# Performance work log

Hardware: AMD Instinct MI355X
Metric: run time of the kernel (lower is better)

Reference implementation:

```python
import jax, jax.numpy as jnp
import numpy as np

B, T, D, NH = 2, 2048, 1024, 32
HD = D // NH  # 32
EPS = 1e-6


def rms_norm(x):
    # normalize over head dim in fp32, cast back
    ms = jnp.mean(x.astype(jnp.float32) ** 2, axis=-1, keepdims=True)
    return x * jax.lax.rsqrt(ms + EPS).astype(x.dtype)


def apply_rope(x, cos, sin):
    d = x.shape[-1] // 2
    x1, x2 = x[..., :d], x[..., d:]
    c = cos[: x.shape[-2], :d]
    s = sin[: x.shape[-2], :d]
    return jnp.concatenate([x1 * c - x2 * s, x2 * c + x1 * s], axis=-1)


def setup_inputs() -> dict:
    key = jax.random.key(0)
    ks = jax.random.split(key, 5)
    sc = 1.0 / np.sqrt(D)
    x = jax.random.normal(ks[0], (B, T, D), jnp.float32)
    Wq = jax.random.normal(ks[1], (D, D), jnp.float32) * sc
    Wk = jax.random.normal(ks[2], (NH * HD, D), jnp.float32) * sc
    Wv = jax.random.normal(ks[3], (NH * HD, D), jnp.float32) * sc
    Wproj = jax.random.normal(ks[4], (D, D), jnp.float32) * sc
    q_gain = jnp.ones((NH,), jnp.float32)  # qk_gain = 1.0
    # real RoPE tables, shape [T, HD//2]
    pos = np.arange(T, dtype=np.float32)
    inv = 1.0 / (10000.0 ** (np.arange(HD // 2, dtype=np.float32) / (HD // 2)))
    ang = pos[:, None] * inv[None, :]
    cos = jnp.asarray(np.cos(ang), jnp.float32)
    sin = jnp.asarray(np.sin(ang), jnp.float32)
    return {"x": x, "Wq": Wq, "Wk": Wk, "Wv": Wv, "Wproj": Wproj,
            "q_gain": q_gain, "cos": cos, "sin": sin}


def reference(x, Wq, Wk, Wv, Wproj, q_gain, cos, sin):
    Bx, Tx, Dx = x.shape
    nh = q_gain.shape[0]
    hd = Dx // nh
    # projections -> [B, H, T, hd]
    q = (x @ Wq.T).reshape(Bx, Tx, nh, hd).transpose(0, 2, 1, 3)
    k = (x @ Wk.T).reshape(Bx, Tx, nh, hd).transpose(0, 2, 1, 3)
    v = (x @ Wv.T).reshape(Bx, Tx, nh, hd).transpose(0, 2, 1, 3)
    q = apply_rope(rms_norm(q), cos, sin) * q_gain[None, :, None, None]
    k = apply_rope(rms_norm(k), cos, sin)
    scale = hd ** (-0.5)
    scores = jnp.einsum('bhqd,bhkd->bhqk', q, k) * scale
    causal = jnp.tril(jnp.ones((Tx, Tx), bool))
    scores = jnp.where(causal, scores, jnp.finfo(scores.dtype).min)
    attn = jax.nn.softmax(scores, axis=-1)
    y = jnp.einsum('bhqk,bhkd->bhqd', attn, v)
    y = y.transpose(0, 2, 1, 3).reshape(Bx, Tx, Dx)
    return y @ Wproj.T
```

## Files before the change

### kernel.cpp

```cpp
#include <hip/hip_runtime.h>

#define DEV __device__ __forceinline__

typedef __bf16 bf16x8 __attribute__((ext_vector_type(8)));
typedef float f32x4 __attribute__((ext_vector_type(4)));

static constexpr int Tn = 2048;
static constexpr int Dn = 1024;
static constexpr int NHn = 32;
static constexpr int Mn = 2 * Tn;
static constexpr float QSCALE = 0.17677669529663687f * 1.4426950408889634f;

DEV unsigned short f2bf(float f) {
    unsigned int u = __builtin_bit_cast(unsigned int, f);
    u = u + 0x7FFFu + ((u >> 16) & 1u);
    return (unsigned short)(u >> 16);
}

#define GPTR(p) ((const __attribute__((address_space(1))) void*)(p))
#define LPTR(p) ((__attribute__((address_space(3))) void*)(p))

__global__ __launch_bounds__(256) void cast_all(
    const float* __restrict__ x, const float* __restrict__ Wq, const float* __restrict__ Wk,
    const float* __restrict__ Wv, const float* __restrict__ Wp,
    unsigned short* __restrict__ xb, unsigned short* __restrict__ wall) {
    int i = blockIdx.x * 256 + threadIdx.x;
    const float* src;
    ushort4* dst;
    if (i < (1 << 20)) {
        src = x + (size_t)i * 4;
        dst = reinterpret_cast<ushort4*>(xb) + i;
    } else {
        int j = i - (1 << 20);
        int sel = j >> 18, off = j & ((1 << 18) - 1);
        const float* w = (sel == 0) ? Wq : (sel == 1) ? Wk : (sel == 2) ? Wv : Wp;
        src = w + (size_t)off * 4;
        dst = reinterpret_cast<ushort4*>(wall) + ((size_t)sel << 18) + off;
    }
    float4 v = *reinterpret_cast<const float4*>(src);
    ushort4 o;
    o.x = f2bf(v.x); o.y = f2bf(v.y); o.z = f2bf(v.z); o.w = f2bf(v.w);
    *dst = o;
}

__global__ __launch_bounds__(256) void gemm_qkv(
    const unsigned short* __restrict__ A, const unsigned short* __restrict__ Wall,
    unsigned short* __restrict__ Qn, unsigned short* __restrict__ Kn, unsigned short* __restrict__ Vt,
    const float* __restrict__ gain, const float* __restrict__ cosp, const float* __restrict__ sinp) {
    const int z = blockIdx.z;
    const unsigned short* Bm = Wall + (size_t)z * (Dn * Dn);
    const int m0 = blockIdx.x * 128, n0 = blockIdx.y * 128;
    const int tid = threadIdx.x, w = tid >> 6, l = tid & 63;
    const int wm = w & 1, wn = w >> 1, lm = l & 15, quad = l >> 4;

    __shared__ __align__(16) unsigned short As[128 * 32];
    __shared__ __align__(16) unsigned short Bs[128 * 32];

    f32x4 acc[4][4] = {};

    const int r0 = (w * 2 + 0) * 16 + (l >> 2);
    const int r1 = (w * 2 + 1) * 16 + (l >> 2);
    const int c0 = (l & 3) * 8;
    const unsigned short* gA0 = A + (long)(m0 + r0) * Dn + c0;
    const unsigned short* gA1 = A + (long)(m0 + r1) * Dn + c0;
    const unsigned short* gB0 = Bm + (long)(n0 + r0) * Dn + c0;
    const unsigned short* gB1 = Bm + (long)(n0 + r1) * Dn + c0;
    unsigned short* lA0 = As + (w * 2 + 0) * 16 * 32;
    unsigned short* lA1 = As + (w * 2 + 1) * 16 * 32;
    unsigned short* lB0 = Bs + (w * 2 + 0) * 16 * 32;
    unsigned short* lB1 = Bs + (w * 2 + 1) * 16 * 32;

    for (int kk = 0; kk < Dn; kk += 32) {
        __builtin_amdgcn_global_load_lds(GPTR(gA0 + kk), LPTR(lA0), 16, 0, 0);
        __builtin_amdgcn_global_load_lds(GPTR(gA1 + kk), LPTR(lA1), 16, 0, 0);
        __builtin_amdgcn_global_load_lds(GPTR(gB0 + kk), LPTR(lB0), 16, 0, 0);
        __builtin_amdgcn_global_load_lds(GPTR(gB1 + kk), LPTR(lB1), 16, 0, 0);
        __syncthreads();
        bf16x8 af[4], bfv[4];
#pragma unroll
        for (int mt = 0; mt < 4; ++mt)
            af[mt] = __builtin_bit_cast(bf16x8,
                *reinterpret_cast<const uint4*>(As + (wm * 64 + mt * 16 + lm) * 32 + quad * 8));
#pragma unroll
        for (int nt = 0; nt < 4; ++nt)
            bfv[nt] = __builtin_bit_cast(bf16x8,
                *reinterpret_cast<const uint4*>(Bs + (wn * 64 + nt * 16 + lm) * 32 + quad * 8));
#pragma unroll
        for (int mt = 0; mt < 4; ++mt)
#pragma unroll
            for (int nt = 0; nt < 4; ++nt)
                acc[mt][nt] = __builtin_amdgcn_mfma_f32_16x16x32_bf16(af[mt], bfv[nt], acc[mt][nt], 0, 0, 0);
        __syncthreads();
    }

    if (z == 2) {
#pragma unroll
        for (int mt = 0; mt < 4; ++mt) {
            int row0 = m0 + wm * 64 + mt * 16 + quad * 4;
            int b_ = row0 >> 11, t_ = row0 & (Tn - 1);
#pragma unroll
            for (int nt = 0; nt < 4; ++nt) {
                int col = n0 + wn * 64 + nt * 16 + lm;
                int hh = col >> 5, dd = col & 31;
                ushort4 o4;
                o4.x = f2bf(acc[mt][nt][0]); o4.y = f2bf(acc[mt][nt][1]);
                o4.z = f2bf(acc[mt][nt][2]); o4.w = f2bf(acc[mt][nt][3]);
                *reinterpret_cast<ushort4*>(&Vt[((long)(b_ * NHn + hh) * 32 + dd) * Tn + t_]) = o4;
            }
        }
    } else {
        unsigned short* dst = z ? Kn : Qn;
#pragma unroll
        for (int mt = 0; mt < 4; ++mt)
#pragma unroll
            for (int r = 0; r < 4; ++r) {
                int row = m0 + wm * 64 + mt * 16 + quad * 4 + r;
                int b_ = row >> 11, t_ = row & (Tn - 1);
                float c = cosp[t_ * 16 + lm], s = sinp[t_ * 16 + lm];
#pragma unroll
                for (int g = 0; g < 2; ++g) {
                    float x1 = acc[mt][2 * g][r], x2 = acc[mt][2 * g + 1][r];
                    float ssv = x1 * x1 + x2 * x2;
#pragma unroll
                    for (int off = 8; off >= 1; off >>= 1) ssv += __shfl_xor(ssv, off, 16);
                    float rinv = rsqrtf(ssv * (1.0f / 32.0f) + 1e-6f);
                    x1 *= rinv; x2 *= rinv;
                    float o1 = x1 * c - x2 * s;
                    float o2 = x2 * c + x1 * s;
                    int hh = (n0 + wn * 64 + g * 32) >> 5;
                    if (z == 0) { float gs = gain[hh] * QSCALE; o1 *= gs; o2 *= gs; }
                    long base = ((long)(b_ * NHn + hh) * Tn + t_) * 32;
                    dst[base + lm] = f2bf(o1);
                    dst[base + 16 + lm] = f2bf(o2);
                }
            }
    }
}

__global__ __launch_bounds__(256) void gemm_proj(
    const unsigned short* __restrict__ A, const unsigned short* __restrict__ Bm,
    float* __restrict__ C) {
    const int m0 = blockIdx.x * 128, n0 = blockIdx.y * 128;
    const int tid = threadIdx.x, w = tid >> 6, l = tid & 63;
    const int wm = w & 1, wn = w >> 1, lm = l & 15, quad = l >> 4;

    __shared__ __align__(16) unsigned short As[128 * 32];
    __shared__ __align__(16) unsigned short Bs[128 * 32];

    f32x4 acc[4][4] = {};

    const int r0 = (w * 2 + 0) * 16 + (l >> 2);
    const int r1 = (w * 2 + 1) * 16 + (l >> 2);
    const int c0 = (l & 3) * 8;
    const unsigned short* gA0 = A + (long)(m0 + r0) * Dn + c0;
    const unsigned short* gA1 = A + (long)(m0 + r1) * Dn + c0;
    const unsigned short* gB0 = Bm + (long)(n0 + r0) * Dn + c0;
    const unsigned short* gB1 = Bm + (long)(n0 + r1) * Dn + c0;
    unsigned short* lA0 = As + (w * 2 + 0) * 16 * 32;
    unsigned short* lA1 = As + (w * 2 + 1) * 16 * 32;
    unsigned short* lB0 = Bs + (w * 2 + 0) * 16 * 32;
    unsigned short* lB1 = Bs + (w * 2 + 1) * 16 * 32;

    for (int kk = 0; kk < Dn; kk += 32) {
        __builtin_amdgcn_global_load_lds(GPTR(gA0 + kk), LPTR(lA0), 16, 0, 0);
        __builtin_amdgcn_global_load_lds(GPTR(gA1 + kk), LPTR(lA1), 16, 0, 0);
        __builtin_amdgcn_global_load_lds(GPTR(gB0 + kk), LPTR(lB0), 16, 0, 0);
        __builtin_amdgcn_global_load_lds(GPTR(gB1 + kk), LPTR(lB1), 16, 0, 0);
        __syncthreads();
        bf16x8 af[4], bfv[4];
#pragma unroll
        for (int mt = 0; mt < 4; ++mt)
            af[mt] = __builtin_bit_cast(bf16x8,
                *reinterpret_cast<const uint4*>(As + (wm * 64 + mt * 16 + lm) * 32 + quad * 8));
#pragma unroll
        for (int nt = 0; nt < 4; ++nt)
            bfv[nt] = __builtin_bit_cast(bf16x8,
                *reinterpret_cast<const uint4*>(Bs + (wn * 64 + nt * 16 + lm) * 32 + quad * 8));
#pragma unroll
        for (int mt = 0; mt < 4; ++mt)
#pragma unroll
            for (int nt = 0; nt < 4; ++nt)
                acc[mt][nt] = __builtin_amdgcn_mfma_f32_16x16x32_bf16(af[mt], bfv[nt], acc[mt][nt], 0, 0, 0);
        __syncthreads();
    }
#pragma unroll
    for (int mt = 0; mt < 4; ++mt)
#pragma unroll
        for (int nt = 0; nt < 4; ++nt)
#pragma unroll
            for (int r = 0; r < 4; ++r) {
                int rg = m0 + wm * 64 + mt * 16 + quad * 4 + r;
                int cg = n0 + wn * 64 + nt * 16 + lm;
                C[(long)rg * Dn + cg] = acc[mt][nt][r];
            }
}

__global__ __launch_bounds__(256) void attn(
    const unsigned short* __restrict__ Qn, const unsigned short* __restrict__ Kn,
    const unsigned short* __restrict__ Vt, unsigned short* __restrict__ Y) {
    const int bx = blockIdx.x, h = blockIdx.y, b = blockIdx.z;
    const int tid = threadIdx.x, w = tid >> 6, l = tid & 63;
    const int lm = l & 15, quad = l >> 4;
    const long bh = b * NHn + h;
    const unsigned short* Qh = Qn + bh * Tn * 32;
    const unsigned short* Kh = Kn + bh * Tn * 32;
    const unsigned short* Vh = Vt + bh * 32 * Tn;
    __shared__ __align__(16) unsigned short Pl[4][16][76];
    unsigned short* Pw = &Pl[w][0][0];

    for (int pass = 0; pass < 2; ++pass) {
        const int qb = pass ? (15 - bx) : bx;
        const int q0 = qb * 128 + w * 32;

        bf16x8 qf[2];
        float negM[2][4];
        float lpart[2][4] = {};
        f32x4 o[2][2] = {{{0.f, 0.f, 0.f, 0.f}, {0.f, 0.f, 0.f, 0.f}},
                         {{0.f, 0.f, 0.f, 0.f}, {0.f, 0.f, 0.f, 0.f}}};
#pragma unroll
        for (int t = 0; t < 2; ++t) {
            qf[t] = __builtin_bit_cast(bf16x8,
                *reinterpret_cast<const uint4*>(Qh + (q0 + t * 16 + lm) * 32 + quad * 8));
            float ss = 0.f;
#pragma unroll
            for (int j = 0; j < 8; ++j) { float v = (float)qf[t][j]; ss += v * v; }
            ss += __shfl_xor(ss, 16);
            ss += __shfl_xor(ss, 32);
            float Mv = __builtin_sqrtf(ss * 32.0f);
#pragma unroll
            for (int r = 0; r < 4; ++r) negM[t][r] = -__shfl(Mv, quad * 4 + r, 16);
        }

        const int kend = q0 + 31;
        uint4 ka[4], va[4], kb2[4], vb2[4];

        auto load_t = [&](uint4* kd, uint4* vd, int k0) {
#pragma unroll
            for (int i = 0; i < 4; ++i)
                kd[i] = *reinterpret_cast<const uint4*>(Kh + (k0 + i * 16 + lm) * 32 + quad * 8);
#pragma unroll
            for (int kf2 = 0; kf2 < 2; ++kf2)
#pragma unroll
                for (int nh_ = 0; nh_ < 2; ++nh_)
                    vd[kf2 * 2 + nh_] = *reinterpret_cast<const uint4*>(
                        Vh + (nh_ * 16 + lm) * Tn + k0 + kf2 * 32 + quad * 8);
        };

        auto compute_t = [&](const uint4* kd, const uint4* vd, int k0) {
#pragma unroll
            for (int t = 0; t < 2; ++t) {
                if (k0 > q0 + t * 16 + 15) continue;
                f32x4 s[4];
#pragma unroll
                for (int i = 0; i < 4; ++i) {
                    f32x4 zz = {0.f, 0.f, 0.f, 0.f};
                    s[i] = __builtin_amdgcn_mfma_f32_16x16x32_bf16(
                        qf[t], __builtin_bit_cast(bf16x8, kd[i]), zz, 0, 0, 0);
                }
                const bool full = (k0 + 63) <= (q0 + t * 16);
#pragma unroll
                for (int r = 0; r < 4; ++r) {
                    const int qrow = q0 + t * 16 + quad * 4 + r;
                    const float nm = negM[t][r];
                    float ls = lpart[t][r];
#pragma unroll
                    for (int i = 0; i < 4; ++i) {
                        float p = __builtin_amdgcn_exp2f(s[i][r] + nm);
                        if (!full) {
                            int kc = k0 + i * 16 + lm;
                            p = (kc <= qrow) ? p : 0.0f;
                        }
                        s[i][r] = p;
                        ls += p;
                    }
                    lpart[t][r] = ls;
                }
#pragma unroll
                for (int i = 0; i < 4; ++i)
#pragma unroll
                    for (int r = 0; r < 4; ++r)
                        Pw[(quad * 4 + r) * 76 + i * 16 + lm] = f2bf(s[i][r]);
#pragma unroll
                for (int kf2 = 0; kf2 < 2; ++kf2) {
                    bf16x8 pf = __builtin_bit_cast(bf16x8,
                        *reinterpret_cast<const uint4*>(Pw + lm * 76 + kf2 * 32 + quad * 8));
#pragma unroll
                    for (int nh_ = 0; nh_ < 2; ++nh_)
                        o[t][nh_] = __builtin_amdgcn_mfma_f32_16x16x32_bf16(
                            pf, __builtin_bit_cast(bf16x8, vd[kf2 * 2 + nh_]), o[t][nh_], 0, 0, 0);
                }
            }
        };

        load_t(ka, va, 0);
        int k0 = 0;
        while (true) {
            int nk = k0 + 64;
            if (nk <= kend) load_t(kb2, vb2, nk);
            compute_t(ka, va, k0);
            if (nk > kend) break;
            k0 = nk;
            nk = k0 + 64;
            if (nk <= kend) load_t(ka, va, nk);
            compute_t(kb2, vb2, k0);
            if (nk > kend) break;
            k0 = nk;
        }

#pragma unroll
        for (int t = 0; t < 2; ++t)
#pragma unroll
            for (int r = 0; r < 4; ++r) {
                float ls = lpart[t][r];
#pragma unroll
                for (int off = 8; off >= 1; off >>= 1) ls += __shfl_xor(ls, off, 16);
                float inv = 1.0f / ls;
                int qrow = q0 + t * 16 + quad * 4 + r;
                long base = ((long)(b * Tn + qrow) * NHn + h) * 32;
                Y[base + lm] = f2bf(o[t][0][r] * inv);
                Y[base + 16 + lm] = f2bf(o[t][1][r] * inv);
            }
    }
}

extern "C" void kernel_launch(void* const* d_in, const int* in_sizes, int n_in,
                              void* d_out, int out_size, void* d_ws, size_t ws_size,
                              hipStream_t stream) {
    (void)in_sizes; (void)n_in; (void)out_size; (void)ws_size;
    const float* x = (const float*)d_in[0];
    const float* Wq = (const float*)d_in[1];
    const float* Wk = (const float*)d_in[2];
    const float* Wv = (const float*)d_in[3];
    const float* Wp = (const float*)d_in[4];
    const float* gain = (const float*)d_in[5];
    const float* cosp = (const float*)d_in[6];
    const float* sinp = (const float*)d_in[7];

    char* ws = (char*)d_ws;
    const size_t SZ = (size_t)Mn * Dn * 2;
    unsigned short* xb = (unsigned short*)ws;
    unsigned short* wall = (unsigned short*)(ws + SZ);
    unsigned short* qn = (unsigned short*)(ws + 2 * SZ);
    unsigned short* kn = qn + (size_t)Mn * Dn;
    unsigned short* vt = kn + (size_t)Mn * Dn;
    unsigned short* ybuf = vt + (size_t)Mn * Dn;

    cast_all<<<8192, 256, 0, stream>>>(x, Wq, Wk, Wv, Wp, xb, wall);

    gemm_qkv<<<dim3(Mn / 128, Dn / 128, 3), 256, 0, stream>>>(
        xb, wall, qn, kn, vt, gain, cosp, sinp);

    attn<<<dim3(8, NHn, 2), 256, 0, stream>>>(qn, kn, vt, ybuf);

    gemm_proj<<<dim3(Mn / 128, Dn / 128), 256, 0, stream>>>(
        ybuf, wall + (size_t)3 * Dn * Dn, (float*)d_out);
}
```

Baseline: 213.4 us.

## Shrink attention query tile to 16 rows per wave and double the grid

The attention kernel now gives each wave 16 query rows instead of 32 and each block 64 rows instead of 128, and doubles the grid to 16x32x2 blocks. The row-max offset is folded into the QK MFMA accumulator input, which removes an add before each exp2. Launch bounds now request 4 blocks per CU, and the bf16 conversion uses the compiler's native cast. The aim is more parallelism, better occupancy and less causal load imbalance, at the cost of reloading K/V twice as often per query row.

```diff
diff --git a/kernel.cpp b/kernel.cpp
--- a/kernel.cpp
+++ b/kernel.cpp
@@ -12,9 +12,7 @@
 static constexpr float QSCALE = 0.17677669529663687f * 1.4426950408889634f;
 
 DEV unsigned short f2bf(float f) {
-    unsigned int u = __builtin_bit_cast(unsigned int, f);
-    u = u + 0x7FFFu + ((u >> 16) & 1u);
-    return (unsigned short)(u >> 16);
+    return __builtin_bit_cast(unsigned short, (__bf16)f);
 }
 
 #define GPTR(p) ((const __attribute__((address_space(1))) void*)(p))
@@ -195,7 +193,7 @@
             }
 }
 
-__global__ __launch_bounds__(256) void attn(
+__global__ __launch_bounds__(256, 4) void attn(
     const unsigned short* __restrict__ Qn, const unsigned short* __restrict__ Kn,
     const unsigned short* __restrict__ Vt, unsigned short* __restrict__ Y) {
     const int bx = blockIdx.x, h = blockIdx.y, b = blockIdx.z;
@@ -209,29 +207,25 @@
     unsigned short* Pw = &Pl[w][0][0];
 
     for (int pass = 0; pass < 2; ++pass) {
-        const int qb = pass ? (15 - bx) : bx;
-        const int q0 = qb * 128 + w * 32;
-
-        bf16x8 qf[2];
-        float negM[2][4];
-        float lpart[2][4] = {};
-        f32x4 o[2][2] = {{{0.f, 0.f, 0.f, 0.f}, {0.f, 0.f, 0.f, 0.f}},
-                         {{0.f, 0.f, 0.f, 0.f}, {0.f, 0.f, 0.f, 0.f}}};
-#pragma unroll
-        for (int t = 0; t < 2; ++t) {
-            qf[t] = __builtin_bit_cast(bf16x8,
-                *reinterpret_cast<const uint4*>(Qh + (q0 + t * 16 + lm) * 32 + quad * 8));
-            float ss = 0.f;
-#pragma unroll
-            for (int j = 0; j < 8; ++j) { float v = (float)qf[t][j]; ss += v * v; }
-            ss += __shfl_xor(ss, 16);
-            ss += __shfl_xor(ss, 32);
-            float Mv = __builtin_sqrtf(ss * 32.0f);
-#pragma unroll
-            for (int r = 0; r < 4; ++r) negM[t][r] = -__shfl(Mv, quad * 4 + r, 16);
-        }
-
-        const int kend = q0 + 31;
+        const int qt = pass ? (31 - bx) : bx;
+        const int q0 = qt * 64 + w * 16;
+
+        bf16x8 qf = __builtin_bit_cast(bf16x8,
+            *reinterpret_cast<const uint4*>(Qh + (q0 + lm) * 32 + quad * 8));
+        float ss = 0.f;
+#pragma unroll
+        for (int j = 0; j < 8; ++j) { float v = (float)qf[j]; ss += v * v; }
+        ss += __shfl_xor(ss, 16);
+        ss += __shfl_xor(ss, 32);
+        float Mv = __builtin_sqrtf(ss * 32.0f);
+        f32x4 negM;
+#pragma unroll
+        for (int r = 0; r < 4; ++r) negM[r] = -__shfl(Mv, quad * 4 + r, 16);
+
+        float lpart[4] = {};
+        f32x4 o[2] = {{0.f, 0.f, 0.f, 0.f}, {0.f, 0.f, 0.f, 0.f}};
+
+        const int kend = q0 + 15;
         uint4 ka[4], va[4], kb2[4], vb2[4];
 
         auto load_t = [&](uint4* kd, uint4* vd, int k0) {
@@ -247,48 +241,41 @@
         };
 
         auto compute_t = [&](const uint4* kd, const uint4* vd, int k0) {
-#pragma unroll
-            for (int t = 0; t < 2; ++t) {
-                if (k0 > q0 + t * 16 + 15) continue;
-                f32x4 s[4];
+            f32x4 s[4];
+#pragma unroll
+            for (int i = 0; i < 4; ++i)
+                s[i] = __builtin_amdgcn_mfma_f32_16x16x32_bf16(
+                    qf, __builtin_bit_cast(bf16x8, kd[i]), negM, 0, 0, 0);
+            const bool full = (k0 + 63) <= q0;
+#pragma unroll
+            for (int r = 0; r < 4; ++r) {
+                const int qrow = q0 + quad * 4 + r;
+                float ls = lpart[r];
 #pragma unroll
                 for (int i = 0; i < 4; ++i) {
-                    f32x4 zz = {0.f, 0.f, 0.f, 0.f};
-                    s[i] = __builtin_amdgcn_mfma_f32_16x16x32_bf16(
-                        qf[t], __builtin_bit_cast(bf16x8, kd[i]), zz, 0, 0, 0);
+                    float p = __builtin_amdgcn_exp2f(s[i][r]);
+                    if (!full) {
+                        int kc = k0 + i * 16 + lm;
+                        p = (kc <= qrow) ? p : 0.0f;
+                    }
+                    s[i][r] = p;
+                    ls += p;
                 }
-                const bool full = (k0 + 63) <= (q0 + t * 16);
-#pragma unroll
-                for (int r = 0; r < 4; ++r) {
-                    const int qrow = q0 + t * 16 + quad * 4 + r;
-                    const float nm = negM[t][r];
-                    float ls = lpart[t][r];
-#pragma unroll
-                    for (int i = 0; i < 4; ++i) {
-                        float p = __builtin_amdgcn_exp2f(s[i][r] + nm);
-                        if (!full) {
-                            int kc = k0 + i * 16 + lm;
-                            p = (kc <= qrow) ? p : 0.0f;
-                        }
-                        s[i][r] = p;
-                        ls += p;
-                    }
-                    lpart[t][r] = ls;
-                }
-#pragma unroll
-                for (int i = 0; i < 4; ++i)
-#pragma unroll
-                    for (int r = 0; r < 4; ++r)
-                        Pw[(quad * 4 + r) * 76 + i * 16 + lm] = f2bf(s[i][r]);
-#pragma unroll
-                for (int kf2 = 0; kf2 < 2; ++kf2) {
-                    bf16x8 pf = __builtin_bit_cast(bf16x8,
-                        *reinterpret_cast<const uint4*>(Pw + lm * 76 + kf2 * 32 + quad * 8));
-#pragma unroll
-                    for (int nh_ = 0; nh_ < 2; ++nh_)
-                        o[t][nh_] = __builtin_amdgcn_mfma_f32_16x16x32_bf16(
-                            pf, __builtin_bit_cast(bf16x8, vd[kf2 * 2 + nh_]), o[t][nh_], 0, 0, 0);
-                }
+                lpart[r] = ls;
+            }
+#pragma unroll
+            for (int i = 0; i < 4; ++i)
+#pragma unroll
+                for (int r = 0; r < 4; ++r)
+                    Pw[(quad * 4 + r) * 76 + i * 16 + lm] = f2bf(s[i][r]);
+#pragma unroll
+            for (int kf2 = 0; kf2 < 2; ++kf2) {
+                bf16x8 pf = __builtin_bit_cast(bf16x8,
+                    *reinterpret_cast<const uint4*>(Pw + lm * 76 + kf2 * 32 + quad * 8));
+#pragma unroll
+                for (int nh_ = 0; nh_ < 2; ++nh_)
+                    o[nh_] = __builtin_amdgcn_mfma_f32_16x16x32_bf16(
+                        pf, __builtin_bit_cast(bf16x8, vd[kf2 * 2 + nh_]), o[nh_], 0, 0, 0);
             }
         };
 
@@ -308,18 +295,16 @@
         }
 
 #pragma unroll
-        for (int t = 0; t < 2; ++t)
-#pragma unroll
-            for (int r = 0; r < 4; ++r) {
-                float ls = lpart[t][r];
-#pragma unroll
-                for (int off = 8; off >= 1; off >>= 1) ls += __shfl_xor(ls, off, 16);
-                float inv = 1.0f / ls;
-                int qrow = q0 + t * 16 + quad * 4 + r;
-                long base = ((long)(b * Tn + qrow) * NHn + h) * 32;
-                Y[base + lm] = f2bf(o[t][0][r] * inv);
-                Y[base + 16 + lm] = f2bf(o[t][1][r] * inv);
-            }
+        for (int r = 0; r < 4; ++r) {
+            float ls = lpart[r];
+#pragma unroll
+            for (int off = 8; off >= 1; off >>= 1) ls += __shfl_xor(ls, off, 16);
+            float inv = 1.0f / ls;
+            int qrow = q0 + quad * 4 + r;
+            long base = ((long)(b * Tn + qrow) * NHn + h) * 32;
+            Y[base + lm] = f2bf(o[0][r] * inv);
+            Y[base + 16 + lm] = f2bf(o[1][r] * inv);
+        }
     }
 }
 
@@ -350,7 +335,7 @@
     gemm_qkv<<<dim3(Mn / 128, Dn / 128, 3), 256, 0, stream>>>(
         xb, wall, qn, kn, vt, gain, cosp, sinp);
 
-    attn<<<dim3(8, NHn, 2), 256, 0, stream>>>(qn, kn, vt, ybuf);
+    attn<<<dim3(16, NHn, 2), 256, 0, stream>>>(qn, kn, vt, ybuf);
 
     gemm_proj<<<dim3(Mn / 128, Dn / 128), 256, 0, stream>>>(
         ybuf, wall + (size_t)3 * Dn * Dn, (float*)d_out);
```

New measurement: 270.8 us. +26.9%, slower.

## Split attention key range across two wave groups and merge partials in LDS

Applied to the files above, without the earlier changes.

The attention kernel now launches 512 threads per block. Two groups of four waves each process half of the causal key tiles for the same query rows, and the partial outputs and row sums are combined through shared memory before the write. The per-row max subtraction is folded into the MFMA accumulator init, and f2bf uses the native bf16 conversion. This raises parallelism per block to shorten the critical path of long causal rows. The cost is extra shared memory and two block barriers per pass.

```diff
diff --git a/kernel.cpp b/kernel.cpp
--- a/kernel.cpp
+++ b/kernel.cpp
@@ -12,9 +12,7 @@
 static constexpr float QSCALE = 0.17677669529663687f * 1.4426950408889634f;
 
 DEV unsigned short f2bf(float f) {
-    unsigned int u = __builtin_bit_cast(unsigned int, f);
-    u = u + 0x7FFFu + ((u >> 16) & 1u);
-    return (unsigned short)(u >> 16);
+    return __builtin_bit_cast(unsigned short, (__bf16)f);
 }
 
 #define GPTR(p) ((const __attribute__((address_space(1))) void*)(p))
@@ -195,25 +193,27 @@
             }
 }
 
-__global__ __launch_bounds__(256) void attn(
+__global__ __launch_bounds__(512, 4) void attn(
     const unsigned short* __restrict__ Qn, const unsigned short* __restrict__ Kn,
     const unsigned short* __restrict__ Vt, unsigned short* __restrict__ Y) {
     const int bx = blockIdx.x, h = blockIdx.y, b = blockIdx.z;
     const int tid = threadIdx.x, w = tid >> 6, l = tid & 63;
+    const int wq = w & 3, kg = w >> 2;
     const int lm = l & 15, quad = l >> 4;
     const long bh = b * NHn + h;
     const unsigned short* Qh = Qn + bh * Tn * 32;
     const unsigned short* Kh = Kn + bh * Tn * 32;
     const unsigned short* Vh = Vt + bh * 32 * Tn;
-    __shared__ __align__(16) unsigned short Pl[4][16][76];
+    __shared__ __align__(16) unsigned short Pl[8][16][76];
+    __shared__ float Po[4][64][25];
     unsigned short* Pw = &Pl[w][0][0];
 
     for (int pass = 0; pass < 2; ++pass) {
         const int qb = pass ? (15 - bx) : bx;
-        const int q0 = qb * 128 + w * 32;
+        const int q0 = qb * 128 + wq * 32;
 
         bf16x8 qf[2];
-        float negM[2][4];
+        f32x4 negC[2];
         float lpart[2][4] = {};
         f32x4 o[2][2] = {{{0.f, 0.f, 0.f, 0.f}, {0.f, 0.f, 0.f, 0.f}},
                          {{0.f, 0.f, 0.f, 0.f}, {0.f, 0.f, 0.f, 0.f}}};
@@ -228,10 +228,14 @@
             ss += __shfl_xor(ss, 32);
             float Mv = __builtin_sqrtf(ss * 32.0f);
 #pragma unroll
-            for (int r = 0; r < 4; ++r) negM[t][r] = -__shfl(Mv, quad * 4 + r, 16);
-        }
-
-        const int kend = q0 + 31;
+            for (int r = 0; r < 4; ++r) negC[t][r] = -__shfl(Mv, quad * 4 + r, 16);
+        }
+
+        const int ntiles = (q0 >> 6) + 1;
+        const int nsplit = ntiles >> 1;
+        const int ts = kg ? nsplit : 0;
+        const int te = kg ? ntiles : nsplit;
+
         uint4 ka[4], va[4], kb2[4], vb2[4];
 
         auto load_t = [&](uint4* kd, uint4* vd, int k0) {
@@ -252,20 +256,17 @@
                 if (k0 > q0 + t * 16 + 15) continue;
                 f32x4 s[4];
 #pragma unroll
-                for (int i = 0; i < 4; ++i) {
-                    f32x4 zz = {0.f, 0.f, 0.f, 0.f};
+                for (int i = 0; i < 4; ++i)
                     s[i] = __builtin_amdgcn_mfma_f32_16x16x32_bf16(
-                        qf[t], __builtin_bit_cast(bf16x8, kd[i]), zz, 0, 0, 0);
-                }
+                        qf[t], __builtin_bit_cast(bf16x8, kd[i]), negC[t], 0, 0, 0);
                 const bool full = (k0 + 63) <= (q0 + t * 16);
 #pragma unroll
                 for (int r = 0; r < 4; ++r) {
                     const int qrow = q0 + t * 16 + quad * 4 + r;
-                    const float nm = negM[t][r];
                     float ls = lpart[t][r];
 #pragma unroll
                     for (int i = 0; i < 4; ++i) {
-                        float p = __builtin_amdgcn_exp2f(s[i][r] + nm);
+                        float p = __builtin_amdgcn_exp2f(s[i][r]);
                         if (!full) {
                             int kc = k0 + i * 16 + lm;
                             p = (kc <= qrow) ? p : 0.0f;
@@ -292,34 +293,55 @@
             }
         };
 
-        load_t(ka, va, 0);
-        int k0 = 0;
-        while (true) {
-            int nk = k0 + 64;
-            if (nk <= kend) load_t(kb2, vb2, nk);
-            compute_t(ka, va, k0);
-            if (nk > kend) break;
-            k0 = nk;
-            nk = k0 + 64;
-            if (nk <= kend) load_t(ka, va, nk);
-            compute_t(kb2, vb2, k0);
-            if (nk > kend) break;
-            k0 = nk;
-        }
-
-#pragma unroll
-        for (int t = 0; t < 2; ++t)
-#pragma unroll
-            for (int r = 0; r < 4; ++r) {
-                float ls = lpart[t][r];
-#pragma unroll
-                for (int off = 8; off >= 1; off >>= 1) ls += __shfl_xor(ls, off, 16);
-                float inv = 1.0f / ls;
-                int qrow = q0 + t * 16 + quad * 4 + r;
-                long base = ((long)(b * Tn + qrow) * NHn + h) * 32;
-                Y[base + lm] = f2bf(o[t][0][r] * inv);
-                Y[base + 16 + lm] = f2bf(o[t][1][r] * inv);
-            }
+        if (te > ts) {
+            int k0 = ts * 64;
+            const int kendv = (te - 1) * 64;
+            load_t(ka, va, k0);
+            while (true) {
+                int nk = k0 + 64;
+                if (nk <= kendv) load_t(kb2, vb2, nk);
+                compute_t(ka, va, k0);
+                if (nk > kendv) break;
+                k0 = nk;
+                nk = k0 + 64;
+                if (nk <= kendv) load_t(ka, va, nk);
+                compute_t(kb2, vb2, k0);
+                if (nk > kendv) break;
+                k0 = nk;
+            }
+        }
+
+        if (kg) {
+            float* p = &Po[wq][l][0];
+#pragma unroll
+            for (int t = 0; t < 2; ++t)
+#pragma unroll
+                for (int nh_ = 0; nh_ < 2; ++nh_)
+#pragma unroll
+                    for (int r = 0; r < 4; ++r) p[(t * 2 + nh_) * 4 + r] = o[t][nh_][r];
+#pragma unroll
+            for (int t = 0; t < 2; ++t)
+#pragma unroll
+                for (int r = 0; r < 4; ++r) p[16 + t * 4 + r] = lpart[t][r];
+        }
+        __syncthreads();
+        if (!kg) {
+            const float* p = &Po[wq][l][0];
+#pragma unroll
+            for (int t = 0; t < 2; ++t)
+#pragma unroll
+                for (int r = 0; r < 4; ++r) {
+                    float ls = lpart[t][r] + p[16 + t * 4 + r];
+#pragma unroll
+                    for (int off = 8; off >= 1; off >>= 1) ls += __shfl_xor(ls, off, 16);
+                    float inv = 1.0f / ls;
+                    int qrow = q0 + t * 16 + quad * 4 + r;
+                    long base = ((long)(b * Tn + qrow) * NHn + h) * 32;
+                    Y[base + lm] = f2bf((o[t][0][r] + p[(t * 2 + 0) * 4 + r]) * inv);
+                    Y[base + 16 + lm] = f2bf((o[t][1][r] + p[(t * 2 + 1) * 4 + r]) * inv);
+                }
+        }
+        __syncthreads();
     }
 }
 
@@ -350,7 +372,7 @@
     gemm_qkv<<<dim3(Mn / 128, Dn / 128, 3), 256, 0, stream>>>(
         xb, wall, qn, kn, vt, gain, cosp, sinp);
 
-    attn<<<dim3(8, NHn, 2), 256, 0, stream>>>(qn, kn, vt, ybuf);
+    attn<<<dim3(8, NHn, 2), 512, 0, stream>>>(qn, kn, vt, ybuf);
 
     gemm_proj<<<dim3(Mn / 128, Dn / 128), 256, 0, stream>>>(
         ybuf, wall + (size_t)3 * Dn * Dn, (float*)d_out);
```

Measured after the change: 307.6 us. 1.44x slower.
